# Performance work log

Measured on AMD Instinct MI355X. Metric: run time of the kernel, lower is better.

Reference implementation:

```python
import jax, jax.numpy as jnp
import numpy as np

B, T, E, H, L = 2, 2048, 1024, 16, 4
HD = E // H
FF = 4 * E


def setup_inputs() -> dict:
    key = jax.random.key(0)
    ks = jax.random.split(key, 9)
    s = 0.02
    return {
        "x": jax.random.normal(ks[0], (B, T, E), dtype=jnp.float32),
        "Wqkv": jax.random.normal(ks[1], (L, E, 3 * E), dtype=jnp.float32) * s,
        "bqkv": jnp.zeros((L, 3 * E), dtype=jnp.float32),
        "Wproj": jax.random.normal(ks[2], (L, E, E), dtype=jnp.float32) * s,
        "bproj": jnp.zeros((L, E), dtype=jnp.float32),
        "W1": jax.random.normal(ks[3], (L, E, FF), dtype=jnp.float32) * s,
        "b1": jnp.zeros((L, FF), dtype=jnp.float32),
        "W2": jax.random.normal(ks[4], (L, FF, E), dtype=jnp.float32) * s,
        "b2": jnp.zeros((L, E), dtype=jnp.float32),
    }


def _attention(x, Wqkv_l, bqkv_l, Wproj_l, bproj_l):
    # (B,T,E) -> (B,T,E); manual softmax attention as in source
    qkv = x @ Wqkv_l + bqkv_l                      # (B,T,3E)
    q, k, v = jnp.split(qkv, 3, axis=-1)
    q = q.reshape(B, T, H, HD).transpose(0, 2, 1, 3)  # (B,H,T,HD)
    k = k.reshape(B, T, H, HD).transpose(0, 2, 1, 3)
    v = v.reshape(B, T, H, HD).transpose(0, 2, 1, 3)
    att = jnp.einsum("bhqd,bhkd->bhqk", q, k) * (1.0 / np.sqrt(HD))
    att = jax.nn.softmax(att, axis=-1)             # (B,H,T,T)
    y = jnp.einsum("bhqk,bhkd->bhqd", att, v)      # (B,H,T,HD)
    y = y.transpose(0, 2, 1, 3).reshape(B, T, E)
    return y @ Wproj_l + bproj_l


def reference(x, Wqkv, bqkv, Wproj, bproj, W1, b1, W2, b2):
    for l in range(L):
        x = x + _attention(x, Wqkv[l], bqkv[l], Wproj[l], bproj[l])  # residual x+f(x)
        h = jax.nn.gelu(x @ W1[l] + b1[l]) @ W2[l] + b2[l]           # MLP block
        x = x + h
    return x
```

## Files before the change

kernel.cpp:

```cpp
#include <hip/hip_runtime.h>
#include <hip/hip_bf16.h>

#define B_  2
#define T_  2048
#define E_  1024
#define H_  16
#define HD_ 64
#define FF_ 4096
#define L_  4
#define M_  (B_*T_)
#define RS_ (3*E_)

typedef unsigned short u16;
typedef __attribute__((ext_vector_type(8))) short  short8;
typedef __attribute__((ext_vector_type(4))) float  f32x4;

#define QS 0.18033688011112042f

__device__ __forceinline__ u16 f2bf(float f) {
    union { float f; unsigned u; } v; v.f = f;
    unsigned r = (v.u + 0x7fffu + ((v.u >> 16) & 1u)) >> 16;
    return (u16)r;
}
__device__ __forceinline__ u16 f2bf_trunc(float f) {
    union { float f; unsigned u; } v; v.f = f;
    return (u16)(v.u >> 16);
}

__device__ __forceinline__ void gll16(const u16* g, u16* lds) {
    __builtin_amdgcn_global_load_lds(
        (const __attribute__((address_space(1))) unsigned int*)g,
        (__attribute__((address_space(3))) unsigned int*)lds, 16, 0, 0);
}

__global__ __launch_bounds__(256) void transpose_weights(
    const float* __restrict__ Wqkv, const float* __restrict__ Wproj,
    const float* __restrict__ W1,   const float* __restrict__ W2,
    u16* __restrict__ WT) {
    __shared__ float tile[32][33];
    int bid = blockIdx.x;
    const float* src; u16* dst; int K, N, lt;
    if (bid < 3072)      { src = Wqkv;  dst = WT;           K = 1024; N = 3072; lt = bid;        }
    else if (bid < 4096) { src = Wproj; dst = WT + 3145728; K = 1024; N = 1024; lt = bid - 3072; }
    else if (bid < 8192) { src = W1;    dst = WT + 4194304; K = 1024; N = 4096; lt = bid - 4096; }
    else                 { src = W2;    dst = WT + 8388608; K = 4096; N = 1024; lt = bid - 8192; }
    int tpr = N >> 5;
    int ti = lt / tpr, tj = lt % tpr;
    int k0 = ti << 5, n0 = tj << 5;
    int tx = threadIdx.x & 31, ty = threadIdx.x >> 5;
    for (int i = 0; i < 4; i++) {
        int r = ty + (i << 3);
        tile[r][tx] = src[(size_t)(k0 + r) * N + n0 + tx];
    }
    __syncthreads();
    for (int i = 0; i < 4; i++) {
        int r = ty + (i << 3);
        dst[(size_t)(n0 + r) * K + k0 + tx] = f2bf(tile[tx][r]);
    }
}

__global__ __launch_bounds__(256) void convert_kernel(
    const float* __restrict__ in, u16* __restrict__ out, int n4) {
    int i = blockIdx.x * 256 + threadIdx.x;
    if (i < n4) {
        float4 v = ((const float4*)in)[i];
        ushort4 w;
        w.x = f2bf(v.x); w.y = f2bf(v.y); w.z = f2bf(v.z); w.w = f2bf(v.w);
        ((ushort4*)out)[i] = w;
    }
}

template <int EPI>
__global__ __launch_bounds__(512, 4) void gemm_fat(
    const u16* __restrict__ A, const u16* __restrict__ Bt,
    const float* __restrict__ bias, u16* __restrict__ outp,
    int N, int K) {
    __shared__ u16 As[3][128 * 32];
    __shared__ u16 Bs[3][256 * 32];
    int t = threadIdx.x;
    int wid = t >> 6, lane = t & 63;
    int l15 = t & 15, quad = (t >> 4) & 3;
    int wr = wid >> 2, wc = wid & 3;

    int nbx = N >> 8;
    int nwg = nbx << 5;
    int flat = blockIdx.x;
    int q = nwg >> 3;
    int gid = (flat & 7) * q + (flat >> 3);
    int within = gid & 127;
    int m0 = (within >> 2) << 7;
    int n0 = (((gid >> 7) << 2) + (within & 3)) << 8;

    f32x4 acc[4][4];
#pragma unroll
    for (int i = 0; i < 4; i++)
#pragma unroll
        for (int j = 0; j < 4; j++) acc[i][j] = (f32x4){0.f, 0.f, 0.f, 0.f};

    int srow = t >> 2;
    int kch  = (((lane & 3) ^ ((lane >> 3) & 3)) << 3);
    const u16* gA  = &A [(size_t)(m0 + srow) * K + kch];
    const u16* gB0 = &Bt[(size_t)(n0 + srow) * K + kch];
    const u16* gB1 = gB0 + (size_t)128 * K;

    int xo = (l15 >> 1) & 3;
    int abase = (((wr << 6) + l15) << 5) + ((quad ^ xo) << 3);
    int bbase = (((wc << 6) + l15) << 5) + ((quad ^ xo) << 3);

    int nk = K >> 5;

#define STAGE_FAT(buf, ko) do {                                              \
        gll16(gA  + (ko), &As[buf][(wid << 4) << 5]);                        \
        gll16(gB0 + (ko), &Bs[buf][(wid << 4) << 5]);                        \
        gll16(gB1 + (ko), &Bs[buf][((wid << 4) + 128) << 5]);                \
    } while (0)

    STAGE_FAT(0, 0);
    STAGE_FAT(1, 32);

    for (int kk = 0; kk < nk; kk++) {
        if (kk < nk - 1) asm volatile("s_waitcnt vmcnt(3)" ::: "memory");
        else             asm volatile("s_waitcnt vmcnt(0)" ::: "memory");
        __builtin_amdgcn_s_barrier();
        __builtin_amdgcn_sched_barrier(0);

        if (kk + 2 < nk) STAGE_FAT((kk + 2) % 3, (kk + 2) << 5);

        const u16* as = &As[kk % 3][0];
        const u16* bs = &Bs[kk % 3][0];
        short8 af[4], bfr[4];
#pragma unroll
        for (int i = 0; i < 4; i++)
            af[i] = *(const short8*)(as + abase + (i << 9));
#pragma unroll
        for (int j = 0; j < 4; j++)
            bfr[j] = *(const short8*)(bs + bbase + (j << 9));
#pragma unroll
        for (int i = 0; i < 4; i++)
#pragma unroll
            for (int j = 0; j < 4; j++)
                acc[i][j] = __builtin_amdgcn_mfma_f32_16x16x32_bf16(af[i], bfr[j], acc[i][j], 0, 0, 0);
    }
#undef STAGE_FAT

#pragma unroll
    for (int j = 0; j < 4; j++) {
        int gn = n0 + (wc << 6) + (j << 4) + l15;
        float bv = bias[gn];
#pragma unroll
        for (int i = 0; i < 4; i++) {
            int mb = m0 + (wr << 6) + (i << 4) + (quad << 2);
#pragma unroll
            for (int r = 0; r < 4; r++) {
                size_t idx = (size_t)(mb + r) * N + gn;
                float v = acc[i][j][r] + bv;
                if (EPI == 0) {
                    if (gn < E_) v *= QS;
                    outp[idx] = f2bf(v);
                } else {
                    float u  = 0.7978845608028654f * (v + 0.044715f * v * v * v);
                    float th = 1.f - 2.f / (__expf(2.f * u) + 1.f);
                    outp[idx] = f2bf(0.5f * v * (1.f + th));
                }
            }
        }
    }
}

template <int EPI>
__global__ __launch_bounds__(256, 3) void gemm_sq(
    const u16* __restrict__ A, const u16* __restrict__ Bt,
    const float* __restrict__ bias, u16* __restrict__ outp,
    int N, int K) {
    __shared__ u16 As[3][128 * 32];
    __shared__ u16 Bs[3][128 * 32];
    int t = threadIdx.x;
    int wid = t >> 6, lane = t & 63;
    int l15 = t & 15, quad = (t >> 4) & 3;
    int wr = wid >> 1, wc = wid & 1;

    int nbx = N >> 7;
    int nwg = nbx << 5;
    int flat = blockIdx.x;
    int q = nwg >> 3;
    int gid = (flat & 7) * q + (flat >> 3);
    int within = gid & 127;
    int m0 = (within >> 2) << 7;
    int n0 = (((gid >> 7) << 2) + (within & 3)) << 7;

    f32x4 acc[4][4];
#pragma unroll
    for (int i = 0; i < 4; i++)
#pragma unroll
        for (int j = 0; j < 4; j++) acc[i][j] = (f32x4){0.f, 0.f, 0.f, 0.f};

    int kch = (((lane & 3) ^ ((lane >> 3) & 3)) << 3);
    const u16* gA = &A [(size_t)(m0 + (wid << 5) + (lane >> 2)) * K + kch];
    const u16* gB = &Bt[(size_t)(n0 + (wid << 5) + (lane >> 2)) * K + kch];

    int xo = (l15 >> 1) & 3;
    int abase = (((wr << 6) + l15) << 5) + ((quad ^ xo) << 3);
    int bbase = (((wc << 6) + l15) << 5) + ((quad ^ xo) << 3);

    int nk = K >> 5;

#define STAGE_SQ(buf, ko) do {                                                \
        gll16(gA + (ko),                  &As[buf][((wid << 5)     ) << 5]);  \
        gll16(gA + (ko) + (size_t)16 * K, &As[buf][((wid << 5) + 16) << 5]);  \
        gll16(gB + (ko),                  &Bs[buf][((wid << 5)     ) << 5]);  \
        gll16(gB + (ko) + (size_t)16 * K, &Bs[buf][((wid << 5) + 16) << 5]);  \
    } while (0)

    STAGE_SQ(0, 0);
    STAGE_SQ(1, 32);

    for (int kk = 0; kk < nk; kk++) {
        if (kk < nk - 1) asm volatile("s_waitcnt vmcnt(4)" ::: "memory");
        else             asm volatile("s_waitcnt vmcnt(0)" ::: "memory");
        __builtin_amdgcn_s_barrier();
        __builtin_amdgcn_sched_barrier(0);

        if (kk + 2 < nk) STAGE_SQ((kk + 2) % 3, (kk + 2) << 5);

        const u16* as = &As[kk % 3][0];
        const u16* bs = &Bs[kk % 3][0];
        short8 af[4], bfr[4];
#pragma unroll
        for (int i = 0; i < 4; i++)
            af[i] = *(const short8*)(as + abase + (i << 9));
#pragma unroll
        for (int j = 0; j < 4; j++)
            bfr[j] = *(const short8*)(bs + bbase + (j << 9));
#pragma unroll
        for (int i = 0; i < 4; i++)
#pragma unroll
            for (int j = 0; j < 4; j++)
                acc[i][j] = __builtin_amdgcn_mfma_f32_16x16x32_bf16(af[i], bfr[j], acc[i][j], 0, 0, 0);
    }
#undef STAGE_SQ

#pragma unroll
    for (int j = 0; j < 4; j++) {
        int gn = n0 + (wc << 6) + (j << 4) + l15;
        float bv = bias[gn];
#pragma unroll
        for (int i = 0; i < 4; i++) {
            int mb = m0 + (wr << 6) + (i << 4) + (quad << 2);
#pragma unroll
            for (int r = 0; r < 4; r++) {
                size_t idx = (size_t)(mb + r) * N + gn;
                float v = acc[i][j][r] + bv;
                if (EPI == 0) {
                    if (gn < E_) v *= QS;
                    outp[idx] = f2bf(v);
                } else {
                    float u  = 0.7978845608028654f * (v + 0.044715f * v * v * v);
                    float th = 1.f - 2.f / (__expf(2.f * u) + 1.f);
                    outp[idx] = f2bf(0.5f * v * (1.f + th));
                }
            }
        }
    }
}

__global__ __launch_bounds__(512, 4) void gemm_n64_sk(
    const u16* __restrict__ A, const u16* __restrict__ Bt,
    const float* __restrict__ bias, const float* __restrict__ res,
    float* __restrict__ outp, u16* __restrict__ out2, int N, int K) {
    __shared__ u16 As[2][3][128 * 32];
    __shared__ u16 Bs[2][3][64 * 32];
    int t = threadIdx.x;
    int wid = t >> 6, lane = t & 63;
    int grp = wid >> 2, w4 = wid & 3;
    int l15 = t & 15, quad = (t >> 4) & 3;
    int wr = w4 >> 1, wc = w4 & 1;

    int flat = blockIdx.x;
    int gid = ((flat & 7) << 6) + (flat >> 3);
    int within = gid & 127;
    int m0 = (within >> 2) << 7;
    int n0 = (((gid >> 7) << 2) + (within & 3)) << 6;

    f32x4 acc[4][2];
#pragma unroll
    for (int i = 0; i < 4; i++)
#pragma unroll
        for (int j = 0; j < 2; j++) acc[i][j] = (f32x4){0.f, 0.f, 0.f, 0.f};

    int kh = K >> 1;
    int kch = (((lane & 3) ^ ((lane >> 3) & 3)) << 3);
    const u16* gA = &A [(size_t)(m0 + (w4 << 5) + (lane >> 2)) * K + (size_t)grp * kh + kch];
    const u16* gB = &Bt[(size_t)(n0 + (w4 << 4) + (lane >> 2)) * K + (size_t)grp * kh + kch];

    int xo = (l15 >> 1) & 3;
    int abase = (((wr << 6) + l15) << 5) + ((quad ^ xo) << 3);
    int bbase = (((wc << 5) + l15) << 5) + ((quad ^ xo) << 3);

    int nk = kh >> 5;

#define STAGE_SK(buf, ko) do {                                                 \
        gll16(gA + (ko),                  &As[grp][buf][((w4 << 5)     ) << 5]); \
        gll16(gA + (ko) + (size_t)16 * K, &As[grp][buf][((w4 << 5) + 16) << 5]); \
        gll16(gB + (ko),                  &Bs[grp][buf][((w4 << 4)     ) << 5]); \
    } while (0)

    STAGE_SK(0, 0);
    STAGE_SK(1, 32);

    for (int kk = 0; kk < nk; kk++) {
        if (kk < nk - 1) asm volatile("s_waitcnt vmcnt(3)" ::: "memory");
        else             asm volatile("s_waitcnt vmcnt(0)" ::: "memory");
        __builtin_amdgcn_s_barrier();
        __builtin_amdgcn_sched_barrier(0);

        if (kk + 2 < nk) STAGE_SK((kk + 2) % 3, (kk + 2) << 5);

        const u16* as = &As[grp][kk % 3][0];
        const u16* bs = &Bs[grp][kk % 3][0];
        short8 af[4], bfr[2];
#pragma unroll
        for (int i = 0; i < 4; i++)
            af[i] = *(const short8*)(as + abase + (i << 9));
#pragma unroll
        for (int j = 0; j < 2; j++)
            bfr[j] = *(const short8*)(bs + bbase + (j << 9));
#pragma unroll
        for (int i = 0; i < 4; i++)
#pragma unroll
            for (int j = 0; j < 2; j++)
                acc[i][j] = __builtin_amdgcn_mfma_f32_16x16x32_bf16(
                    af[i], bfr[j], acc[i][j], 0, 0, 0);
    }
#undef STAGE_SK

    float* part = (float*)&As[1][0][0];
    int ti = t & 255;
    __syncthreads();
#pragma unroll
    for (int half = 0; half < 2; half++) {
        if (grp == 1) {
#pragma unroll
            for (int i2 = 0; i2 < 2; i2++)
#pragma unroll
                for (int j = 0; j < 2; j++)
                    *(f32x4*)&part[(ti << 4) + (i2 << 3) + (j << 2)] =
                        acc[(half << 1) + i2][j];
        }
        __syncthreads();
        if (grp == 0) {
#pragma unroll
            for (int i2 = 0; i2 < 2; i2++) {
                int i = (half << 1) + i2;
#pragma unroll
                for (int j = 0; j < 2; j++) {
                    f32x4 p = *(const f32x4*)&part[(ti << 4) + (i2 << 3) + (j << 2)];
                    int gn = n0 + (wc << 5) + (j << 4) + l15;
                    float bv = bias[gn];
                    int mb = m0 + (wr << 6) + (i << 4) + (quad << 2);
#pragma unroll
                    for (int r = 0; r < 4; r++) {
                        size_t idx = (size_t)(mb + r) * N + gn;
                        float o = acc[i][j][r] + p[r] + bv + res[idx];
                        outp[idx] = o;
                        out2[idx] = f2bf(o);
                    }
                }
            }
        }
        __syncthreads();
    }
}

__global__ __launch_bounds__(256) void attn_kernel(
    const u16* __restrict__ qkv, u16* __restrict__ y) {
    __shared__ u16 Ks[2][64 * 64];
    __shared__ u16 Vt[2][64 * 64];
    __shared__ u16 Pb[4][16 * 64];

    int t = threadIdx.x;
    int q0 = blockIdx.x << 6;
    int h  = blockIdx.y;
    int b  = blockIdx.z;
    const u16* bq = qkv + (size_t)b * T_ * RS_;

    int wid = t >> 6, lane = t & 63, l15 = t & 15, quad = (t >> 4) & 3;
    int sw = l15 & 7;
    int ro0 = (l15 << 6) + ((quad ^ sw) << 3);
    int ro1 = ro0 ^ 32;
    int krow = (wid << 4) + (lane >> 3);
    size_t kg0 = (size_t)krow * RS_ + E_ + h * 64 + (((lane & 7) ^ (lane >> 3)) << 3);
    int vkp = t & 31, vdc = t >> 5;
    size_t vg0 = (size_t)(2 * vkp) * RS_ + 2 * E_ + h * 64 + (vdc << 3);
    int vwo[8];
#pragma unroll
    for (int i = 0; i < 8; i++)
        vwo[i] = (((vdc << 3) + i) << 6) + ((((vkp >> 2) ^ i)) << 3) + ((vkp & 3) << 1);
    int pwo[4];
#pragma unroll
    for (int kt = 0; kt < 4; kt++)
        pwo[kt] = (l15 << 6) + ((((kt << 1) | (quad >> 1)) ^ sw) << 3) + ((quad & 1) << 2);
    u16* pw = &Pb[wid][0];

    const u16* qp = bq + (size_t)(q0 + (wid << 4) + l15) * RS_ + h * 64;
    short8 qf0 = *(const short8*)(qp + (quad << 3));
    short8 qf1 = *(const short8*)(qp + (quad << 3) + 32);

    float l = 0.f;
    f32x4 o[4];
#pragma unroll
    for (int dt = 0; dt < 4; dt++) o[dt] = (f32x4){0.f, 0.f, 0.f, 0.f};

    gll16(bq + kg0,            &Ks[0][(wid << 4) << 6]);
    gll16(bq + kg0 + 8 * RS_,  &Ks[0][((wid << 4) + 8) << 6]);
    {
        union { uint4 q; u16 u[8]; } a_, b_;
        a_.q = *(const uint4*)(bq + vg0);
        b_.q = *(const uint4*)(bq + vg0 + RS_);
#pragma unroll
        for (int i = 0; i < 8; i++) {
            unsigned pk = (unsigned)a_.u[i] | ((unsigned)b_.u[i] << 16);
            *(unsigned*)(&Vt[0][0] + vwo[i]) = pk;
        }
    }

#define ATTN_CHUNK(KSB, VTB, KSN, VTN, C0) do {                                \
    __syncthreads();                           \
    int cn_ = (C0) + 64;                                                       \
    uint4 v0_, v1_;                                                            \
    bool pf_ = (cn_ < T_);                                                     \
    if (pf_) {                                                                 \
        size_t cb_ = (size_t)cn_ * RS_;                                        \
        gll16(bq + cb_ + kg0,           (KSN) + ((wid << 4) << 6));            \
        gll16(bq + cb_ + kg0 + 8 * RS_, (KSN) + (((wid << 4) + 8) << 6));      \
        v0_ = *(const uint4*)(bq + cb_ + vg0);                                 \
        v1_ = *(const uint4*)(bq + cb_ + vg0 + RS_);                           \
    }                                                                          \
    f32x4 s_[4];                                                               \
    _Pragma("unroll")                                                          \
    for (int kt = 0; kt < 4; kt++) {                                           \
        short8 ka0 = *(const short8*)((KSB) + (kt << 10) + ro0);               \
        short8 ka1 = *(const short8*)((KSB) + (kt << 10) + ro1);               \
        f32x4 z = (f32x4){0.f, 0.f, 0.f, 0.f};                                 \
        z = __builtin_amdgcn_mfma_f32_16x16x32_bf16(ka0, qf0, z, 0, 0, 0);     \
        z = __builtin_amdgcn_mfma_f32_16x16x32_bf16(ka1, qf1, z, 0, 0, 0);     \
        s_[kt] = z;                                                            \
    }                                                                          \
    float rsum_ = 0.f;                                                         \
    _Pragma("unroll")                                                          \
    for (int kt = 0; kt < 4; kt++) {                                           \
        float p0_ = __builtin_amdgcn_exp2f(s_[kt][0]);                         \
        float p1_ = __builtin_amdgcn_exp2f(s_[kt][1]);                         \
        float p2_ = __builtin_amdgcn_exp2f(s_[kt][2]);                         \
        float p3_ = __builtin_amdgcn_exp2f(s_[kt][3]);                         \
        rsum_ += (p0_ + p1_) + (p2_ + p3_);                                    \
        ushort4 w_;                                                            \
        w_.x = f2bf_trunc(p0_); w_.y = f2bf_trunc(p1_);                        \
        w_.z = f2bf_trunc(p2_); w_.w = f2bf_trunc(p3_);                        \
        *(ushort4*)(pw + pwo[kt]) = w_;                                        \
    }                                                                          \
    rsum_ += __shfl_xor(rsum_, 16);                                            \
    rsum_ += __shfl_xor(rsum_, 32);                                            \
    l += rsum_;                                                                \
    __threadfence_block();                   \
    short8 pb0 = *(const short8*)(pw + ro0);                                   \
    short8 pb1 = *(const short8*)(pw + ro1);                                   \
    _Pragma("unroll")                                                          \
    for (int dt = 0; dt < 4; dt++) {                                           \
        short8 vf0 = *(const short8*)((VTB) + (dt << 10) + ro0);               \
        short8 vf1 = *(const short8*)((VTB) + (dt << 10) + ro1);               \
        o[dt] = __builtin_amdgcn_mfma_f32_16x16x32_bf16(vf0, pb0, o[dt], 0, 0, 0); \
        o[dt] = __builtin_amdgcn_mfma_f32_16x16x32_bf16(vf1, pb1, o[dt], 0, 0, 0); \
    }                                                                          \
    if (pf_) {                                                                 \
        union { uint4 q; u16 u[8]; } a_, b_;                                   \
        a_.q = v0_; b_.q = v1_;                                                \
        _Pragma("unroll")                                                      \
        for (int i = 0; i < 8; i++) {                                          \
            unsigned pk_ = (unsigned)a_.u[i] | ((unsigned)b_.u[i] << 16);      \
            *(unsigned*)((VTN) + vwo[i]) = pk_;                                \
        }                                                                      \
    }                                                                          \
} while (0)

    for (int c0 = 0; c0 < T_; c0 += 128) {
        ATTN_CHUNK(&Ks[0][0], &Vt[0][0], &Ks[1][0], &Vt[1][0], c0);
        ATTN_CHUNK(&Ks[1][0], &Vt[1][0], &Ks[0][0], &Vt[0][0], c0 + 64);
    }
#undef ATTN_CHUNK

    float rl = __builtin_amdgcn_rcpf(l);
    size_t yrow = ((size_t)b * T_ + q0 + (wid << 4) + l15) * E_ + h * 64;
#pragma unroll
    for (int dt = 0; dt < 4; dt++) {
        ushort4 w;
        w.x = f2bf(o[dt][0] * rl); w.y = f2bf(o[dt][1] * rl);
        w.z = f2bf(o[dt][2] * rl); w.w = f2bf(o[dt][3] * rl);
        *(ushort4*)&y[yrow + (dt << 4) + (quad << 2)] = w;
    }
}

extern "C" void kernel_launch(void* const* d_in, const int* in_sizes, int n_in,
                              void* d_out, int out_size, void* d_ws, size_t ws_size,
                              hipStream_t stream) {
    const float* x_in  = (const float*)d_in[0];
    const float* Wqkv  = (const float*)d_in[1];
    const float* bqkv  = (const float*)d_in[2];
    const float* Wproj = (const float*)d_in[3];
    const float* bproj = (const float*)d_in[4];
    const float* W1    = (const float*)d_in[5];
    const float* b1    = (const float*)d_in[6];
    const float* W2    = (const float*)d_in[7];
    const float* b2    = (const float*)d_in[8];
    float* out = (float*)d_out;

    u16* WT   = (u16*)d_ws;
    u16* qkvb = WT   + 12582912;
    u16* yb   = qkvb + 12582912;
    u16* hb   = yb   + 4194304;
    u16* xb   = hb   + 16777216;

    convert_kernel<<<4096, 256, 0, stream>>>(x_in, xb, M_ * E_ / 4);

    for (int l = 0; l < L_; l++) {
        transpose_weights<<<12288, 256, 0, stream>>>(
            Wqkv + (size_t)l * E_ * 3 * E_, Wproj + (size_t)l * E_ * E_,
            W1 + (size_t)l * E_ * FF_, W2 + (size_t)l * FF_ * E_, WT);

        const float* xcur = (l == 0) ? x_in : out;

        gemm_sq<0><<<dim3(768), 256, 0, stream>>>(
            xb, WT, bqkv + l * 3 * E_, qkvb, 3 * E_, E_);

        attn_kernel<<<dim3(T_ / 64, H_, B_), 256, 0, stream>>>(qkvb, yb);

        gemm_n64_sk<<<dim3(512), 512, 0, stream>>>(
            yb, WT + 3145728, bproj + l * E_, xcur, out, xb, E_, E_);

        gemm_fat<2><<<dim3(512), 512, 0, stream>>>(
            xb, WT + 4194304, b1 + l * FF_, hb, FF_, E_);

        gemm_n64_sk<<<dim3(512), 512, 0, stream>>>(
            hb, WT + 8388608, b2 + l * E_, out, out, xb, E_, FF_);
    }
}
```

Before: 1.138 ms.

## Compute softmax denominator via MFMA, packed bf16 convert, remap attention grid

The attention kernel now computes the softmax row sum with an extra MFMA against a ones vector instead of per-lane adds plus cross-lane shuffles. It packs the probabilities with the v_cvt_pk_bf16_f32 instruction, which rounds rather than truncates. The 3D grid becomes a 1D grid whose index is remapped so that consecutive blocks group head/batch pairs across query tiles, aiming for better K/V cache locality. The denominator is now summed from bf16-rounded probabilities, so it matches the numerator exactly but differs slightly from the old fp32 sum.

```diff
diff --git a/kernel.cpp b/kernel.cpp
--- a/kernel.cpp
+++ b/kernel.cpp
@@ -21,10 +21,6 @@
     union { float f; unsigned u; } v; v.f = f;
     unsigned r = (v.u + 0x7fffu + ((v.u >> 16) & 1u)) >> 16;
     return (u16)r;
-}
-__device__ __forceinline__ u16 f2bf_trunc(float f) {
-    union { float f; unsigned u; } v; v.f = f;
-    return (u16)(v.u >> 16);
 }
 
 __device__ __forceinline__ void gll16(const u16* g, u16* lds) {
@@ -378,9 +374,11 @@
     __shared__ u16 Pb[4][16 * 64];
 
     int t = threadIdx.x;
-    int q0 = blockIdx.x << 6;
-    int h  = blockIdx.y;
-    int b  = blockIdx.z;
+    int bid = blockIdx.x;
+    int bh  = ((bid >> 8) << 3) | (bid & 7);
+    int q0  = ((bid >> 3) & 31) << 6;
+    int h   = bh & 15;
+    int b   = bh >> 4;
     const u16* bq = qkv + (size_t)b * T_ * RS_;
 
     int wid = t >> 6, lane = t & 63, l15 = t & 15, quad = (t >> 4) & 3;
@@ -405,10 +403,14 @@
     short8 qf0 = *(const short8*)(qp + (quad << 3));
     short8 qf1 = *(const short8*)(qp + (quad << 3) + 32);
 
-    float l = 0.f;
+    short8 ones;
+#pragma unroll
+    for (int i = 0; i < 8; i++) ones[i] = (short)0x3F80;
+
     f32x4 o[4];
 #pragma unroll
     for (int dt = 0; dt < 4; dt++) o[dt] = (f32x4){0.f, 0.f, 0.f, 0.f};
+    f32x4 ol = (f32x4){0.f, 0.f, 0.f, 0.f};
 
     gll16(bq + kg0,            &Ks[0][(wid << 4) << 6]);
     gll16(bq + kg0 + 8 * RS_,  &Ks[0][((wid << 4) + 8) << 6]);
@@ -445,22 +447,18 @@
         z = __builtin_amdgcn_mfma_f32_16x16x32_bf16(ka1, qf1, z, 0, 0, 0);     \
         s_[kt] = z;                                                            \
     }                                                                          \
-    float rsum_ = 0.f;                                                         \
     _Pragma("unroll")                                                          \
     for (int kt = 0; kt < 4; kt++) {                                           \
         float p0_ = __builtin_amdgcn_exp2f(s_[kt][0]);                         \
         float p1_ = __builtin_amdgcn_exp2f(s_[kt][1]);                         \
         float p2_ = __builtin_amdgcn_exp2f(s_[kt][2]);                         \
         float p3_ = __builtin_amdgcn_exp2f(s_[kt][3]);                         \
-        rsum_ += (p0_ + p1_) + (p2_ + p3_);                                    \
-        ushort4 w_;                                                            \
-        w_.x = f2bf_trunc(p0_); w_.y = f2bf_trunc(p1_);                        \
-        w_.z = f2bf_trunc(p2_); w_.w = f2bf_trunc(p3_);                        \
-        *(ushort4*)(pw + pwo[kt]) = w_;                                        \
+        unsigned lo_, hi_;                                                     \
+        asm("v_cvt_pk_bf16_f32 %0, %1, %2" : "=v"(lo_) : "v"(p0_), "v"(p1_)); \
+        asm("v_cvt_pk_bf16_f32 %0, %1, %2" : "=v"(hi_) : "v"(p2_), "v"(p3_)); \
+        uint2 w_; w_.x = lo_; w_.y = hi_;                                      \
+        *(uint2*)(pw + pwo[kt]) = w_;                                          \
     }                                                                          \
-    rsum_ += __shfl_xor(rsum_, 16);                                            \
-    rsum_ += __shfl_xor(rsum_, 32);                                            \
-    l += rsum_;                                                                \
     __threadfence_block();                   \
     short8 pb0 = *(const short8*)(pw + ro0);                                   \
     short8 pb1 = *(const short8*)(pw + ro1);                                   \
@@ -471,6 +469,8 @@
         o[dt] = __builtin_amdgcn_mfma_f32_16x16x32_bf16(vf0, pb0, o[dt], 0, 0, 0); \
         o[dt] = __builtin_amdgcn_mfma_f32_16x16x32_bf16(vf1, pb1, o[dt], 0, 0, 0); \
     }                                                                          \
+    ol = __builtin_amdgcn_mfma_f32_16x16x32_bf16(ones, pb0, ol, 0, 0, 0);      \
+    ol = __builtin_amdgcn_mfma_f32_16x16x32_bf16(ones, pb1, ol, 0, 0, 0);      \
     if (pf_) {                                                                 \
         union { uint4 q; u16 u[8]; } a_, b_;                                   \
         a_.q = v0_; b_.q = v1_;                                                \
@@ -488,7 +488,7 @@
     }
 #undef ATTN_CHUNK
 
-    float rl = __builtin_amdgcn_rcpf(l);
+    float rl = __builtin_amdgcn_rcpf(ol[0]);
     size_t yrow = ((size_t)b * T_ + q0 + (wid << 4) + l15) * E_ + h * 64;
 #pragma unroll
     for (int dt = 0; dt < 4; dt++) {
@@ -531,7 +531,7 @@
         gemm_sq<0><<<dim3(768), 256, 0, stream>>>(
             xb, WT, bqkv + l * 3 * E_, qkvb, 3 * E_, E_);
 
-        attn_kernel<<<dim3(T_ / 64, H_, B_), 256, 0, stream>>>(qkvb, yb);
+        attn_kernel<<<dim3(1024), 256, 0, stream>>>(qkvb, yb);
 
         gemm_n64_sk<<<dim3(512), 512, 0, stream>>>(
             yb, WT + 3145728, bproj + l * E_, xcur, out, xb, E_, E_);
```

Result: faster. 1.103 ms (-3.1%).
